# Kernel tuning notes

Hardware: AMD Instinct MI355X
Metric: run time of the kernel (lower is better)

The kernel has to match this reference:

```python
import jax, jax.numpy as jnp
import numpy as np

H = 128
NH = 8
HD = H // NH  # 16
TANH_ALPHA = 10.0
LN_EPS = 1e-5


def _layer_norm(x, g, b):
    mu = jnp.mean(x, axis=-1, keepdims=True)
    var = jnp.mean((x - mu) ** 2, axis=-1, keepdims=True)
    return (x - mu) / jnp.sqrt(var + LN_EPS) * g + b


def setup_inputs() -> dict:
    key = jax.random.key(0)
    ks = jax.random.split(key, 24)
    B, N = 1024, 500

    def p(k, shape):
        return jax.random.normal(k, shape, dtype=jnp.float32) * 0.05

    inp = {
        "node_embeddings": jax.random.normal(ks[0], (B, N, H), jnp.float32),
        "graph_embeddings": jax.random.normal(ks[1], (B, H), jnp.float32),
        "first_node": jax.random.randint(ks[2], (B,), 0, N, jnp.int32),
        "current_node": jax.random.randint(ks[3], (B,), 0, N, jnp.int32),
        "mask": jax.random.randint(ks[4], (B, N), 0, 2, jnp.int32),
        # linear_first: Linear(384, 128)
        "W_first": p(ks[5], (H, 3 * H)),
        "b_first": p(ks[6], (H,)),
        # ln1 / ln2
        "g1": jnp.ones((H,), jnp.float32),
        "beta1": jnp.zeros((H,), jnp.float32),
        "g2": jnp.ones((H,), jnp.float32),
        "beta2": jnp.zeros((H,), jnp.float32),
        # LSTM(128,128) single layer, gate order i,f,g,o
        "W_ih": p(ks[7], (4 * H, H)),
        "W_hh": p(ks[8], (4 * H, H)),
        "b_ih": p(ks[9], (4 * H,)),
        "b_hh": p(ks[10], (4 * H,)),
        # attention / output projections (no bias)
        "Wq": p(ks[11], (H, H)),
        "Wk": p(ks[12], (H, H)),
        "Wv": p(ks[13], (H, H)),
        "Wproj": p(ks[14], (H, H)),
        # logitk: Linear(128,128) with bias
        "Wlk": p(ks[15], (H, H)),
        "blk": p(ks[16], (H,)),
    }
    return inp


def reference(node_embeddings, graph_embeddings, W_first, b_first, g1, beta1,
              W_ih, W_hh, b_ih, b_hh, g2, beta2, Wq, Wk, Wv, Wproj, Wlk, blk,
              first_node, current_node, mask):
    B, N, _ = node_embeddings.shape
    dt = node_embeddings.dtype

    # build_cache: K/V/logitK projections of all node embeddings
    ck = node_embeddings @ Wk.T                # [B,N,128]
    cv = node_embeddings @ Wv.T                # [B,N,128]
    lk = node_embeddings @ Wlk.T + blk         # [B,N,128]

    # context construction
    bidx = jnp.arange(B)
    first_emb = node_embeddings[bidx, first_node]    # [B,128]
    cur_emb = node_embeddings[bidx, current_node]    # [B,128]
    context = jnp.concatenate([graph_embeddings, first_emb, cur_emb], axis=1)
    context = _layer_norm(context @ W_first.T + b_first, g1, beta1)

    # single LSTM step from zero state (build_cache resets h,c to 0)
    gates = context @ W_ih.T + b_ih + b_hh           # h_prev = 0 -> no W_hh term
    i, f, g, o = jnp.split(gates, 4, axis=-1)
    c = jax.nn.sigmoid(i) * jnp.tanh(g)              # c_prev = 0
    h = jax.nn.sigmoid(o) * jnp.tanh(c)
    ctx = _layer_norm(h, g2, beta2)

    # multi-head single-query attention; note (e h) split: head is the FAST dim
    q = (ctx @ Wq.T).reshape(B, HD, NH).transpose(0, 2, 1)       # [B,h,e]
    k = ck.reshape(B, N, HD, NH).transpose(0, 3, 1, 2)           # [B,h,N,e]
    v = cv.reshape(B, N, HD, NH).transpose(0, 3, 1, 2)           # [B,h,N,e]
    maskf = mask.astype(dt)
    scores = jnp.einsum('bhe,bhne->bhn', q, k) / np.sqrt(HD) + maskf[:, None, :]
    att = jax.nn.softmax(scores, axis=-1)
    oh = jnp.einsum('bhn,bhne->bhe', att, v)                     # [B,h,e]
    att_out = oh.reshape(B, H)                                   # (h e): h slow, e fast

    context_emb = att_out @ Wproj.T                              # [B,128]
    comp = jnp.einsum('be,bne->bn', lk, context_emb[:, None, :].squeeze(1)[:, :][None].squeeze(0) if False else context_emb) if False else jnp.einsum('bne,be->bn', lk, context_emb)
    comp = comp / np.sqrt(H)
    comp = TANH_ALPHA * jnp.tanh(comp)
    out = jnp.where(mask == 1, -jnp.inf, comp)
    return out
```

## Files before the change

### kernel.cpp

```cpp
#include <hip/hip_runtime.h>
#include <math.h>

#define NBATCH 1024
#define NNODE  500
#define HDIM   128
#define NHEAD  8
#define G1K    4
#define SPLIT  8
#define PSTRIDE 1040
#define RSQRT_H 0.08838834764831845f
#define MASK_NEG (-1e30f)

__device__ __forceinline__ float wave_sum64(float v) {
    #pragma unroll
    for (int off = 32; off >= 1; off >>= 1) v += __shfl_xor(v, off, 64);
    return v;
}
__device__ __forceinline__ float wave_max64(float v) {
    #pragma unroll
    for (int off = 32; off >= 1; off >>= 1) v = fmaxf(v, __shfl_xor(v, off, 64));
    return v;
}

template<int G>
__device__ __forceinline__ void block_ln(float (&x)[G], const float* __restrict__ gw,
                                         const float* __restrict__ bw,
                                         int t, int lane, int wv, float (*wpart)[G])
{
    float s[G];
    #pragma unroll
    for (int g = 0; g < G; ++g) s[g] = x[g];
    #pragma unroll
    for (int off = 32; off >= 1; off >>= 1) {
        #pragma unroll
        for (int g = 0; g < G; ++g) s[g] += __shfl_xor(s[g], off, 64);
    }
    if (lane == 0) {
        #pragma unroll
        for (int g = 0; g < G; ++g) wpart[wv][g] = s[g];
    }
    __syncthreads();
    float mu[G];
    #pragma unroll
    for (int g = 0; g < G; ++g) mu[g] = (wpart[0][g] + wpart[1][g]) * (1.f/128.f);
    __syncthreads();
    #pragma unroll
    for (int g = 0; g < G; ++g) { float d = x[g] - mu[g]; s[g] = d * d; }
    #pragma unroll
    for (int off = 32; off >= 1; off >>= 1) {
        #pragma unroll
        for (int g = 0; g < G; ++g) s[g] += __shfl_xor(s[g], off, 64);
    }
    if (lane == 0) {
        #pragma unroll
        for (int g = 0; g < G; ++g) wpart[wv][g] = s[g];
    }
    __syncthreads();
    float gv = gw[t], bv = bw[t];
    #pragma unroll
    for (int g = 0; g < G; ++g) {
        float var = (wpart[0][g] + wpart[1][g]) * (1.f/128.f);
        x[g] = (x[g] - mu[g]) / sqrtf(var + 1e-5f) * gv + bv;
    }
    __syncthreads();
}

__global__ __launch_bounds__(128) void k1_context(
    const float* __restrict__ node, const float* __restrict__ graph,
    const int* __restrict__ firstn, const int* __restrict__ curn,
    const float* __restrict__ W_first, const float* __restrict__ b_first,
    const float* __restrict__ g1, const float* __restrict__ beta1,
    const float* __restrict__ W_ih, const float* __restrict__ b_ih,
    const float* __restrict__ b_hh, const float* __restrict__ g2,
    const float* __restrict__ beta2, const float* __restrict__ Wq,
    const float* __restrict__ Wk, float* __restrict__ qW_out)
{
    const int t = threadIdx.x;
    const int lane = t & 63, wv = t >> 6;
    const int b0 = blockIdx.x * G1K;
    __shared__ __align__(16) float ctx[G1K][384];
    __shared__ __align__(16) float bufB[G1K][128];
    __shared__ float wpart[2][G1K];

    #pragma unroll
    for (int g = 0; g < G1K; ++g) {
        int b = b0 + g;
        ctx[g][t]       = graph[b*HDIM + t];
        ctx[g][128 + t] = node[((size_t)b*NNODE + firstn[b])*HDIM + t];
        ctx[g][256 + t] = node[((size_t)b*NNODE + curn[b])*HDIM + t];
    }
    __syncthreads();

    float x[G1K];
    {
        const float4* Wf4 = (const float4*)W_first;
        float bf = b_first[t];
        #pragma unroll
        for (int g = 0; g < G1K; ++g) x[g] = bf;
        for (int j4 = 0; j4 < 96; ++j4) {
            float4 w = Wf4[t*96 + j4];
            #pragma unroll
            for (int g = 0; g < G1K; ++g) {
                float4 c = ((const float4*)ctx[g])[j4];
                x[g] += c.x*w.x + c.y*w.y + c.z*w.z + c.w*w.w;
            }
        }
    }
    block_ln<G1K>(x, g1, beta1, t, lane, wv, wpart);

    #pragma unroll
    for (int g = 0; g < G1K; ++g) bufB[g][t] = x[g];
    __syncthreads();

    float gi[G1K], gg[G1K], go[G1K];
    {
        const float4* Wih4 = (const float4*)W_ih;
        float bi = b_ih[t]       + b_hh[t];
        float bg = b_ih[256 + t] + b_hh[256 + t];
        float bo = b_ih[384 + t] + b_hh[384 + t];
        #pragma unroll
        for (int g = 0; g < G1K; ++g) { gi[g] = bi; gg[g] = bg; go[g] = bo; }
        for (int j4 = 0; j4 < 32; ++j4) {
            float4 wi = Wih4[(size_t)t*32 + j4];
            float4 wg = Wih4[(size_t)(256 + t)*32 + j4];
            float4 wo = Wih4[(size_t)(384 + t)*32 + j4];
            #pragma unroll
            for (int g = 0; g < G1K; ++g) {
                float4 v = ((const float4*)bufB[g])[j4];
                gi[g] += v.x*wi.x + v.y*wi.y + v.z*wi.z + v.w*wi.w;
                gg[g] += v.x*wg.x + v.y*wg.y + v.z*wg.z + v.w*wg.w;
                go[g] += v.x*wo.x + v.y*wo.y + v.z*wo.z + v.w*wo.w;
            }
        }
    }
    #pragma unroll
    for (int g = 0; g < G1K; ++g) {
        float ig = 1.f / (1.f + expf(-gi[g]));
        float cc = ig * tanhf(gg[g]);
        float og = 1.f / (1.f + expf(-go[g]));
        x[g] = og * tanhf(cc);
    }
    block_ln<G1K>(x, g2, beta2, t, lane, wv, wpart);

    #pragma unroll
    for (int g = 0; g < G1K; ++g) bufB[g][t] = x[g];
    __syncthreads();

    float q8[G1K];
    #pragma unroll
    for (int g = 0; g < G1K; ++g) q8[g] = 0.f;
    {
        const float4* Wq4 = (const float4*)Wq;
        for (int j4 = 0; j4 < 32; ++j4) {
            float4 w = Wq4[t*32 + j4];
            #pragma unroll
            for (int g = 0; g < G1K; ++g) {
                float4 v = ((const float4*)bufB[g])[j4];
                q8[g] += v.x*w.x + v.y*w.y + v.z*w.z + v.w*w.w;
            }
        }
    }
    __syncthreads();
    #pragma unroll
    for (int g = 0; g < G1K; ++g) bufB[g][t] = q8[g];
    __syncthreads();

    for (int h = 0; h < NHEAD; ++h) {
        float a[G1K];
        #pragma unroll
        for (int g = 0; g < G1K; ++g) a[g] = 0.f;
        for (int e = 0; e < 16; ++e) {
            float w = Wk[(e*8 + h)*HDIM + t];
            #pragma unroll
            for (int g = 0; g < G1K; ++g) a[g] += bufB[g][e*8 + h] * w;
        }
        #pragma unroll
        for (int g = 0; g < G1K; ++g)
            qW_out[((size_t)(b0 + g)*NHEAD + h)*HDIM + t] = 0.25f * a[g];
    }
}

__global__ __launch_bounds__(256) void k2a_wave(
    const float* __restrict__ node, const int* __restrict__ mask,
    const float* __restrict__ qW, float* __restrict__ part)
{
    const int b   = blockIdx.x >> 3;
    const int s   = blockIdx.x & 7;
    const int tid = threadIdx.x;
    const int w   = tid >> 6;
    const int lane = tid & 63;
    const int rnl = lane >> 2;
    const int dq  = lane & 3;
    const int gn  = s*64 + w*16 + rnl;

    __shared__ __align__(16) float  s_qw[NHEAD*HDIM];
    __shared__ __align__(16) float4 s_tile[4][16*32];
    __shared__ float s_pp[4][NHEAD*16];
    __shared__ float s_ml[4][16];
    __shared__ float s_gml[16];

    ((float4*)s_qw)[tid] = ((const float4*)(qW + (size_t)b*NHEAD*HDIM))[tid];

    float4 R[8];
    float mf = 0.f;
    const bool valid = (gn < NNODE);
    if (valid) {
        const float4* src = (const float4*)(node + ((size_t)b*NNODE + gn)*HDIM) + dq*8;
        #pragma unroll
        for (int k = 0; k < 8; ++k) R[k] = src[k];
        mf = (float)mask[(size_t)b*NNODE + gn];
    } else {
        #pragma unroll
        for (int k = 0; k < 8; ++k) R[k] = make_float4(0.f,0.f,0.f,0.f);
    }
    __syncthreads();

    float sc[NHEAD];
    #pragma unroll
    for (int h = 0; h < NHEAD; ++h) {
        const float4* qh = (const float4*)(s_qw + h*HDIM) + dq*8;
        float t0 = 0.f;
        #pragma unroll
        for (int k = 0; k < 8; ++k) {
            float4 wv = qh[k];
            t0 += R[k].x*wv.x + R[k].y*wv.y + R[k].z*wv.z + R[k].w*wv.w;
        }
        sc[h] = t0;
    }
    #pragma unroll
    for (int h = 0; h < NHEAD; ++h) {
        sc[h] += __shfl_xor(sc[h], 1, 64);
        sc[h] += __shfl_xor(sc[h], 2, 64);
        sc[h] = valid ? sc[h] + mf : -INFINITY;
    }

    float m[NHEAD], l[NHEAD], p[NHEAD];
    #pragma unroll
    for (int h = 0; h < NHEAD; ++h) {
        float mx = sc[h];
        #pragma unroll
        for (int off = 4; off <= 32; off <<= 1) mx = fmaxf(mx, __shfl_xor(mx, off, 64));
        m[h] = mx;
        p[h] = __expf(sc[h] - mx);
        float sm = p[h];
        #pragma unroll
        for (int off = 4; off <= 32; off <<= 1) sm += __shfl_xor(sm, off, 64);
        l[h] = sm;
    }

    float4* tile = s_tile[w];
    #pragma unroll
    for (int k = 0; k < 8; ++k) {
        int q = dq*8 + k;
        tile[rnl*32 + (q ^ rnl)] = R[k];
    }
    if (dq == 0) {
        #pragma unroll
        for (int h = 0; h < NHEAD; ++h) s_pp[w][h*16 + rnl] = p[h];
    }
    if (lane == 0) {
        #pragma unroll
        for (int h = 0; h < NHEAD; ++h) { s_ml[w][h] = m[h]; s_ml[w][8 + h] = l[h]; }
    }

    float4 a4[4];
    #pragma unroll
    for (int j = 0; j < 4; ++j) a4[j] = make_float4(0.f,0.f,0.f,0.f);
    const int h2 = lane >> 3, d16 = lane & 7;
    #pragma unroll 4
    for (int r = 0; r < 16; ++r) {
        float pv = s_pp[w][h2*16 + r];
        #pragma unroll
        for (int j = 0; j < 4; ++j) {
            float4 nv = tile[r*32 + ((d16*4 + j) ^ r)];
            a4[j].x += pv*nv.x; a4[j].y += pv*nv.y;
            a4[j].z += pv*nv.z; a4[j].w += pv*nv.w;
        }
    }
    __syncthreads();

    if (tid < NHEAD) {
        float gm = -INFINITY;
        #pragma unroll
        for (int w4 = 0; w4 < 4; ++w4) gm = fmaxf(gm, s_ml[w4][tid]);
        float lm = 0.f;
        #pragma unroll
        for (int w4 = 0; w4 < 4; ++w4)
            lm += s_ml[w4][8 + tid] * __expf(s_ml[w4][tid] - gm);
        s_gml[tid] = gm; s_gml[8 + tid] = lm;
    }
    #pragma unroll
    for (int j = 0; j < 4; ++j)
        ((float4*)s_tile)[w*256 + h2*32 + d16*4 + j] = a4[j];
    __syncthreads();

    float* pbase = part + (size_t)blockIdx.x * PSTRIDE;
    {
        const int hh = tid >> 5;
        float gm = s_gml[hh];
        float4 tot = make_float4(0.f,0.f,0.f,0.f);
        #pragma unroll
        for (int w4 = 0; w4 < 4; ++w4) {
            float f = __expf(s_ml[w4][hh] - gm);
            float4 v = ((float4*)s_tile)[w4*256 + tid];
            tot.x += f*v.x; tot.y += f*v.y; tot.z += f*v.z; tot.w += f*v.w;
        }
        if (tid < 16) pbase[tid] = s_gml[tid];
        *(float4*)(pbase + 16 + tid*4) = tot;
    }
}

__global__ __launch_bounds__(256) void k2b_reduce(
    const float* __restrict__ part, const float* __restrict__ Wv,
    const float* __restrict__ Wproj, const float* __restrict__ Wlk,
    const float* __restrict__ blk, float* __restrict__ wce_out,
    float* __restrict__ bias_out)
{
    const int b = blockIdx.x;
    const int tid = threadIdx.x;
    __shared__ __align__(16) float s_an[NHEAD*HDIM];
    __shared__ float s_ao[HDIM], s_ce[HDIM];

    {
        const int h = tid >> 5, q = tid & 31;
        const float* pb = part + (size_t)b*SPLIT*PSTRIDE;
        float m[SPLIT], l[SPLIT];
        float gm = -INFINITY;
        #pragma unroll
        for (int s = 0; s < SPLIT; ++s) {
            m[s] = pb[s*PSTRIDE + h];
            l[s] = pb[s*PSTRIDE + 8 + h];
            gm = fmaxf(gm, m[s]);
        }
        float lsum = 0.f;
        float4 tot = make_float4(0.f,0.f,0.f,0.f);
        #pragma unroll
        for (int s = 0; s < SPLIT; ++s) {
            float f = __expf(m[s] - gm);
            lsum += l[s] * f;
            float4 v = *(const float4*)(pb + s*PSTRIDE + 16 + h*HDIM + q*4);
            tot.x += f*v.x; tot.y += f*v.y; tot.z += f*v.z; tot.w += f*v.w;
        }
        float inv = 1.f / lsum;
        tot.x *= inv; tot.y *= inv; tot.z *= inv; tot.w *= inv;
        *(float4*)(s_an + h*HDIM + q*4) = tot;
    }
    __syncthreads();

    if (tid < HDIM) {
        const int c = tid, h = c >> 4, e = c & 15;
        const int row = e*8 + h;
        float oh = 0.f;
        for (int d = 0; d < HDIM; ++d) oh += s_an[h*HDIM + d] * Wv[row*HDIM + d];
        s_ao[c] = oh;
    }
    __syncthreads();
    if (tid < HDIM) {
        const int c = tid;
        float ce = 0.f;
        for (int j = 0; j < HDIM; ++j) ce += s_ao[j] * Wproj[c*HDIM + j];
        s_ce[c] = ce;
    }
    __syncthreads();
    if (tid < HDIM) {
        const int d = tid;
        float w = 0.f;
        for (int c = 0; c < HDIM; ++c) w += s_ce[c] * Wlk[c*HDIM + d];
        wce_out[(size_t)b*HDIM + d] = w * RSQRT_H;
        if (d == 0) {
            float bb = 0.f;
            for (int c = 0; c < HDIM; ++c) bb += s_ce[c] * blk[c];
            bias_out[b] = bb * RSQRT_H;
        }
    }
}

__global__ __launch_bounds__(256) void k2_flash_mono(
    const float* __restrict__ node, const int* __restrict__ mask,
    const float* __restrict__ qW, const float* __restrict__ Wv,
    const float* __restrict__ Wproj, const float* __restrict__ Wlk,
    const float* __restrict__ blk, float* __restrict__ wce_out,
    float* __restrict__ bias_out)
{
    const int b = blockIdx.x;
    const int tid = threadIdx.x;
    const int lane = tid & 63;
    const int wave = tid >> 6;

    __shared__ float4 s_tile[64*32];
    __shared__ __align__(16) float s_qw[NHEAD*HDIM];
    __shared__ float  s_p[NHEAD*64];
    __shared__ float  s_m[NHEAD], s_l[NHEAD], s_c[NHEAD];
    __shared__ float  s_ao[HDIM], s_ce[HDIM];

    ((float4*)s_qw)[tid] = ((const float4*)(qW + (size_t)b*NHEAD*HDIM))[tid];
    if (tid < NHEAD) { s_m[tid] = -INFINITY; s_l[tid] = 0.f; }

    float4 acc[NHEAD];
    #pragma unroll
    for (int h = 0; h < NHEAD; ++h) acc[h] = make_float4(0.f,0.f,0.f,0.f);

    const int sn = tid & 63;
    const int hp = tid >> 6;
    const int sg = tid >> 5;
    const int aq = tid & 31;
    const float* nodeb = node + (size_t)b*NNODE*HDIM;

    for (int tile = 0; tile < 8; ++tile) {
        const int base = tile*64;
        #pragma unroll
        for (int i = 0; i < 8; ++i) {
            int idx = i*256 + tid;
            int r = idx >> 5, qq = idx & 31;
            int gn = base + r;
            float4 v = make_float4(0.f,0.f,0.f,0.f);
            if (gn < NNODE) v = *(const float4*)(nodeb + (size_t)gn*HDIM + qq*4);
            s_tile[r*32 + (qq ^ (r & 31))] = v;
        }
        __syncthreads();
        {
            float s0 = 0.f, s1 = 0.f;
            const int rb = sn*32, sw = sn & 31;
            const float4* qa = (const float4*)(s_qw + hp*HDIM);
            const float4* qb = (const float4*)(s_qw + (hp + 4)*HDIM);
            #pragma unroll 8
            for (int qq = 0; qq < 32; ++qq) {
                float4 nv = s_tile[rb + (qq ^ sw)];
                float4 av = qa[qq];
                float4 bv = qb[qq];
                s0 += nv.x*av.x + nv.y*av.y + nv.z*av.z + nv.w*av.w;
                s1 += nv.x*bv.x + nv.y*bv.y + nv.z*bv.z + nv.w*bv.w;
            }
            int gn = base + sn;
            if (gn < NNODE) {
                float mf = (float)mask[(size_t)b*NNODE + gn];
                s0 += mf; s1 += mf;
            } else { s0 = -INFINITY; s1 = -INFINITY; }
            s_p[hp*64 + sn] = s0;
            s_p[(hp + 4)*64 + sn] = s1;
        }
        __syncthreads();
        for (int hh = wave; hh < NHEAD; hh += 4) {
            float sv = s_p[hh*64 + lane];
            float mx = wave_max64(sv);
            float mO = s_m[hh];
            float mN = fmaxf(mO, mx);
            float pv = __expf(sv - mN);
            s_p[hh*64 + lane] = pv;
            float sm = wave_sum64(pv);
            if (lane == 0) {
                float corr = __expf(mO - mN);
                s_c[hh] = corr;
                s_l[hh] = s_l[hh]*corr + sm;
                s_m[hh] = mN;
            }
        }
        __syncthreads();
        {
            #pragma unroll
            for (int h = 0; h < NHEAD; ++h) {
                float c = s_c[h];
                acc[h].x *= c; acc[h].y *= c; acc[h].z *= c; acc[h].w *= c;
            }
            #pragma unroll
            for (int j = 0; j < 8; ++j) {
                int n = sg*8 + j;
                float4 nv = s_tile[n*32 + (aq ^ (n & 31))];
                #pragma unroll
                for (int h = 0; h < NHEAD; ++h) {
                    float p = s_p[h*64 + n];
                    acc[h].x += p*nv.x; acc[h].y += p*nv.y;
                    acc[h].z += p*nv.z; acc[h].w += p*nv.w;
                }
            }
        }
        __syncthreads();
    }
    #pragma unroll
    for (int h = 0; h < NHEAD; ++h) s_tile[(sg*8 + h)*32 + aq] = acc[h];
    __syncthreads();
    {
        const int h2 = tid >> 5, q2 = tid & 31;
        float4 tot = make_float4(0.f,0.f,0.f,0.f);
        #pragma unroll
        for (int s = 0; s < 8; ++s) {
            float4 v = s_tile[(s*8 + h2)*32 + q2];
            tot.x += v.x; tot.y += v.y; tot.z += v.z; tot.w += v.w;
        }
        float inv = 1.f / s_l[h2];
        tot.x *= inv; tot.y *= inv; tot.z *= inv; tot.w *= inv;
        ((float4*)s_qw)[h2*32 + q2] = tot;
    }
    __syncthreads();
    if (tid < HDIM) {
        const int c = tid, h = c >> 4, e = c & 15;
        const int row = e*8 + h;
        float oh = 0.f;
        for (int d = 0; d < HDIM; ++d) oh += s_qw[h*HDIM + d] * Wv[row*HDIM + d];
        s_ao[c] = oh;
    }
    __syncthreads();
    if (tid < HDIM) {
        const int c = tid;
        float ce = 0.f;
        for (int j = 0; j < HDIM; ++j) ce += s_ao[j] * Wproj[c*HDIM + j];
        s_ce[c] = ce;
    }
    __syncthreads();
    if (tid < HDIM) {
        const int d = tid;
        float w = 0.f;
        for (int c = 0; c < HDIM; ++c) w += s_ce[c] * Wlk[c*HDIM + d];
        wce_out[(size_t)b*HDIM + d] = w * RSQRT_H;
        if (d == 0) {
            float bb = 0.f;
            for (int c = 0; c < HDIM; ++c) bb += s_ce[c] * blk[c];
            bias_out[b] = bb * RSQRT_H;
        }
    }
}

__global__ __launch_bounds__(256) void k3_out(
    const float* __restrict__ node, const int* __restrict__ mask,
    const float* __restrict__ wce, const float* __restrict__ biasv,
    float* __restrict__ out)
{
    const int slot = (int)((blockIdx.x*256u + threadIdx.x) >> 5);
    const int q = threadIdx.x & 31;
    const int b = slot / NNODE;
    const float4 nv = *(const float4*)(node + (size_t)slot*HDIM + q*4);
    const float4 wv = *(const float4*)(wce + (size_t)b*HDIM + q*4);
    float p = nv.x*wv.x + nv.y*wv.y + nv.z*wv.z + nv.w*wv.w;
    #pragma unroll
    for (int off = 16; off >= 1; off >>= 1) p += __shfl_xor(p, off, 32);
    if (q == 0) {
        float v = 10.f * tanhf(p + biasv[b]);
        out[slot] = (mask[slot] == 1) ? MASK_NEG : v;
    }
}

extern "C" void kernel_launch(void* const* d_in, const int* in_sizes, int n_in,
                              void* d_out, int out_size, void* d_ws, size_t ws_size,
                              hipStream_t stream) {
    const float* node    = (const float*)d_in[0];
    const float* graph   = (const float*)d_in[1];
    const int*   firstn  = (const int*)d_in[2];
    const int*   curn    = (const int*)d_in[3];
    const int*   mask    = (const int*)d_in[4];
    const float* W_first = (const float*)d_in[5];
    const float* b_first = (const float*)d_in[6];
    const float* g1      = (const float*)d_in[7];
    const float* beta1   = (const float*)d_in[8];
    const float* g2      = (const float*)d_in[9];
    const float* beta2   = (const float*)d_in[10];
    const float* W_ih    = (const float*)d_in[11];
    const float* b_ih    = (const float*)d_in[13];
    const float* b_hh    = (const float*)d_in[14];
    const float* Wq      = (const float*)d_in[15];
    const float* Wk      = (const float*)d_in[16];
    const float* Wv      = (const float*)d_in[17];
    const float* Wproj   = (const float*)d_in[18];
    const float* Wlk     = (const float*)d_in[19];
    const float* blk     = (const float*)d_in[20];
    float* out = (float*)d_out;

    float* qW    = (float*)d_ws;
    float* wce   = qW + (size_t)NBATCH*NHEAD*HDIM;
    float* biasv = wce + (size_t)NBATCH*HDIM;
    float* part  = biasv + NBATCH;
    const size_t need = ((size_t)NBATCH*NHEAD*HDIM + (size_t)NBATCH*HDIM + NBATCH
                         + (size_t)NBATCH*SPLIT*PSTRIDE) * sizeof(float);

    k1_context<<<NBATCH/G1K, 128, 0, stream>>>(node, graph, firstn, curn,
        W_first, b_first, g1, beta1, W_ih, b_ih, b_hh, g2, beta2, Wq, Wk, qW);
    if (ws_size >= need) {
        k2a_wave<<<NBATCH*SPLIT, 256, 0, stream>>>(node, mask, qW, part);
        k2b_reduce<<<NBATCH, 256, 0, stream>>>(part, Wv, Wproj, Wlk, blk,
            wce, biasv);
    } else {
        k2_flash_mono<<<NBATCH, 256, 0, stream>>>(node, mask, qW, Wv, Wproj,
            Wlk, blk, wce, biasv);
    }
    k3_out<<<(NBATCH*NNODE)/8, 256, 0, stream>>>(node, mask, wce, biasv, out);
}
```

Measured before the change: 245.5 us.

## Split attention into score pass and bf16-copy softmax pass, reuse bf16 nodes in output

Replaces the split-flash attention with a kernel that computes per-head scores and also writes a bf16 copy of the node embeddings. A second kernel then does a full softmax over those scores and the weighted sum on the bf16 copy. The output kernel reads the bf16 copy instead of fp32 nodes. This aims to cut DRAM traffic in the later passes, at the cost of an extra write pass and reduced precision in the attention and output logits.

Result: slower. 313.9 us (+27.9%).

```diff
diff --git a/kernel.cpp b/kernel.cpp
--- a/kernel.cpp
+++ b/kernel.cpp
@@ -6,10 +6,16 @@
 #define HDIM   128
 #define NHEAD  8
 #define G1K    4
-#define SPLIT  8
-#define PSTRIDE 1040
 #define RSQRT_H 0.08838834764831845f
 #define MASK_NEG (-1e30f)
+
+__device__ __forceinline__ unsigned short bf16rne(float f) {
+    unsigned u = __float_as_uint(f);
+    return (unsigned short)((u + 0x7FFFu + ((u >> 16) & 1u)) >> 16);
+}
+__device__ __forceinline__ float bf2f(unsigned short u) {
+    return __uint_as_float(((unsigned)u) << 16);
+}
 
 __device__ __forceinline__ float wave_sum64(float v) {
     #pragma unroll
@@ -180,170 +186,137 @@
     }
 }
 
-__global__ __launch_bounds__(256) void k2a_wave(
+__global__ __launch_bounds__(256) void k2s_score(
     const float* __restrict__ node, const int* __restrict__ mask,
-    const float* __restrict__ qW, float* __restrict__ part)
-{
-    const int b   = blockIdx.x >> 3;
-    const int s   = blockIdx.x & 7;
+    const float* __restrict__ qW, float* __restrict__ scores,
+    unsigned short* __restrict__ nb16)
+{
+    const int blk = blockIdx.x;
+    const int b = blk >> 2;
+    const int qq = blk & 3;
     const int tid = threadIdx.x;
-    const int w   = tid >> 6;
-    const int lane = tid & 63;
-    const int rnl = lane >> 2;
-    const int dq  = lane & 3;
-    const int gn  = s*64 + w*16 + rnl;
-
-    __shared__ __align__(16) float  s_qw[NHEAD*HDIM];
-    __shared__ __align__(16) float4 s_tile[4][16*32];
-    __shared__ float s_pp[4][NHEAD*16];
-    __shared__ float s_ml[4][16];
-    __shared__ float s_gml[16];
+    const int g = tid >> 5, lane32 = tid & 31;
+    __shared__ __align__(16) float s_qw[NHEAD*HDIM];
 
     ((float4*)s_qw)[tid] = ((const float4*)(qW + (size_t)b*NHEAD*HDIM))[tid];
-
-    float4 R[8];
-    float mf = 0.f;
-    const bool valid = (gn < NNODE);
-    if (valid) {
-        const float4* src = (const float4*)(node + ((size_t)b*NNODE + gn)*HDIM) + dq*8;
-        #pragma unroll
-        for (int k = 0; k < 8; ++k) R[k] = src[k];
-        mf = (float)mask[(size_t)b*NNODE + gn];
-    } else {
-        #pragma unroll
-        for (int k = 0; k < 8; ++k) R[k] = make_float4(0.f,0.f,0.f,0.f);
-    }
-    __syncthreads();
-
-    float sc[NHEAD];
-    #pragma unroll
-    for (int h = 0; h < NHEAD; ++h) {
-        const float4* qh = (const float4*)(s_qw + h*HDIM) + dq*8;
-        float t0 = 0.f;
-        #pragma unroll
-        for (int k = 0; k < 8; ++k) {
-            float4 wv = qh[k];
-            t0 += R[k].x*wv.x + R[k].y*wv.y + R[k].z*wv.z + R[k].w*wv.w;
-        }
-        sc[h] = t0;
-    }
-    #pragma unroll
-    for (int h = 0; h < NHEAD; ++h) {
-        sc[h] += __shfl_xor(sc[h], 1, 64);
-        sc[h] += __shfl_xor(sc[h], 2, 64);
-        sc[h] = valid ? sc[h] + mf : -INFINITY;
-    }
-
-    float m[NHEAD], l[NHEAD], p[NHEAD];
-    #pragma unroll
-    for (int h = 0; h < NHEAD; ++h) {
-        float mx = sc[h];
-        #pragma unroll
-        for (int off = 4; off <= 32; off <<= 1) mx = fmaxf(mx, __shfl_xor(mx, off, 64));
-        m[h] = mx;
-        p[h] = __expf(sc[h] - mx);
-        float sm = p[h];
-        #pragma unroll
-        for (int off = 4; off <= 32; off <<= 1) sm += __shfl_xor(sm, off, 64);
-        l[h] = sm;
-    }
-
-    float4* tile = s_tile[w];
-    #pragma unroll
-    for (int k = 0; k < 8; ++k) {
-        int q = dq*8 + k;
-        tile[rnl*32 + (q ^ rnl)] = R[k];
-    }
-    if (dq == 0) {
-        #pragma unroll
-        for (int h = 0; h < NHEAD; ++h) s_pp[w][h*16 + rnl] = p[h];
-    }
-    if (lane == 0) {
-        #pragma unroll
-        for (int h = 0; h < NHEAD; ++h) { s_ml[w][h] = m[h]; s_ml[w][8 + h] = l[h]; }
-    }
-
-    float4 a4[4];
-    #pragma unroll
-    for (int j = 0; j < 4; ++j) a4[j] = make_float4(0.f,0.f,0.f,0.f);
-    const int h2 = lane >> 3, d16 = lane & 7;
-    #pragma unroll 4
-    for (int r = 0; r < 16; ++r) {
-        float pv = s_pp[w][h2*16 + r];
-        #pragma unroll
-        for (int j = 0; j < 4; ++j) {
-            float4 nv = tile[r*32 + ((d16*4 + j) ^ r)];
-            a4[j].x += pv*nv.x; a4[j].y += pv*nv.y;
-            a4[j].z += pv*nv.z; a4[j].w += pv*nv.w;
-        }
-    }
-    __syncthreads();
-
-    if (tid < NHEAD) {
-        float gm = -INFINITY;
-        #pragma unroll
-        for (int w4 = 0; w4 < 4; ++w4) gm = fmaxf(gm, s_ml[w4][tid]);
-        float lm = 0.f;
-        #pragma unroll
-        for (int w4 = 0; w4 < 4; ++w4)
-            lm += s_ml[w4][8 + tid] * __expf(s_ml[w4][tid] - gm);
-        s_gml[tid] = gm; s_gml[8 + tid] = lm;
-    }
-    #pragma unroll
-    for (int j = 0; j < 4; ++j)
-        ((float4*)s_tile)[w*256 + h2*32 + d16*4 + j] = a4[j];
-    __syncthreads();
-
-    float* pbase = part + (size_t)blockIdx.x * PSTRIDE;
-    {
-        const int hh = tid >> 5;
-        float gm = s_gml[hh];
-        float4 tot = make_float4(0.f,0.f,0.f,0.f);
-        #pragma unroll
-        for (int w4 = 0; w4 < 4; ++w4) {
-            float f = __expf(s_ml[w4][hh] - gm);
-            float4 v = ((float4*)s_tile)[w4*256 + tid];
-            tot.x += f*v.x; tot.y += f*v.y; tot.z += f*v.z; tot.w += f*v.w;
-        }
-        if (tid < 16) pbase[tid] = s_gml[tid];
-        *(float4*)(pbase + 16 + tid*4) = tot;
-    }
-}
-
-__global__ __launch_bounds__(256) void k2b_reduce(
-    const float* __restrict__ part, const float* __restrict__ Wv,
-    const float* __restrict__ Wproj, const float* __restrict__ Wlk,
-    const float* __restrict__ blk, float* __restrict__ wce_out,
-    float* __restrict__ bias_out)
-{
-    const int b = blockIdx.x;
-    const int tid = threadIdx.x;
+    __syncthreads();
+
+    const int nstart = qq * 125;
+    for (int it = 0; it < 16; ++it) {
+        int nl = it*8 + g;
+        if (nl < 125) {
+            int gn = nstart + nl;
+            size_t rbase = ((size_t)b*NNODE + gn)*32;
+            float4 nv = ((const float4*)node)[rbase + lane32];
+            float sc[8];
+            #pragma unroll
+            for (int h = 0; h < 8; ++h) {
+                float4 w = ((const float4*)s_qw)[h*32 + lane32];
+                sc[h] = nv.x*w.x + nv.y*w.y + nv.z*w.z + nv.w*w.w;
+            }
+            #pragma unroll
+            for (int off = 1; off <= 16; off <<= 1) {
+                #pragma unroll
+                for (int h = 0; h < 8; ++h) sc[h] += __shfl_xor(sc[h], off, 64);
+            }
+            float v = sc[0];
+            #pragma unroll
+            for (int h = 1; h < 8; ++h) v = ((lane32 & 7) == h) ? sc[h] : v;
+            if (lane32 < 8) {
+                float mf = (float)mask[(size_t)b*NNODE + gn];
+                scores[((size_t)b*NNODE + gn)*8 + lane32] = v + mf;
+            }
+            ushort4 u;
+            u.x = bf16rne(nv.x); u.y = bf16rne(nv.y);
+            u.z = bf16rne(nv.z); u.w = bf16rne(nv.w);
+            ((ushort4*)nb16)[rbase + lane32] = u;
+        }
+    }
+}
+
+__global__ __launch_bounds__(256) void k2w_attn(
+    const float* __restrict__ scores, const unsigned short* __restrict__ nb16,
+    const float* __restrict__ Wv, const float* __restrict__ Wproj,
+    const float* __restrict__ Wlk, const float* __restrict__ blk_,
+    float* __restrict__ wce_out, float* __restrict__ bias_out)
+{
+    const int b = blockIdx.x, tid = threadIdx.x;
+    const int lane = tid & 63, w = tid >> 6;
+    __shared__ __align__(16) float s_p[NNODE*NHEAD];
+    __shared__ float s_red[4][8];
+    __shared__ float s_m[8], s_l[8];
     __shared__ __align__(16) float s_an[NHEAD*HDIM];
     __shared__ float s_ao[HDIM], s_ce[HDIM];
 
     {
-        const int h = tid >> 5, q = tid & 31;
-        const float* pb = part + (size_t)b*SPLIT*PSTRIDE;
-        float m[SPLIT], l[SPLIT];
-        float gm = -INFINITY;
-        #pragma unroll
-        for (int s = 0; s < SPLIT; ++s) {
-            m[s] = pb[s*PSTRIDE + h];
-            l[s] = pb[s*PSTRIDE + 8 + h];
-            gm = fmaxf(gm, m[s]);
-        }
-        float lsum = 0.f;
-        float4 tot = make_float4(0.f,0.f,0.f,0.f);
-        #pragma unroll
-        for (int s = 0; s < SPLIT; ++s) {
-            float f = __expf(m[s] - gm);
-            lsum += l[s] * f;
-            float4 v = *(const float4*)(pb + s*PSTRIDE + 16 + h*HDIM + q*4);
-            tot.x += f*v.x; tot.y += f*v.y; tot.z += f*v.z; tot.w += f*v.w;
-        }
-        float inv = 1.f / lsum;
-        tot.x *= inv; tot.y *= inv; tot.z *= inv; tot.w *= inv;
-        *(float4*)(s_an + h*HDIM + q*4) = tot;
+        const float4* sc4 = (const float4*)(scores + (size_t)b*NNODE*NHEAD);
+        #pragma unroll
+        for (int i = 0; i < 4; ++i) {
+            int idx = i*256 + tid;
+            if (idx < 1000) ((float4*)s_p)[idx] = sc4[idx];
+        }
+    }
+    __syncthreads();
+    float mx[8];
+    #pragma unroll
+    for (int h = 0; h < 8; ++h) mx[h] = -INFINITY;
+    for (int r = tid; r < NNODE; r += 256) {
+        #pragma unroll
+        for (int h = 0; h < 8; ++h) mx[h] = fmaxf(mx[h], s_p[r*8 + h]);
+    }
+    #pragma unroll
+    for (int off = 1; off <= 32; off <<= 1) {
+        #pragma unroll
+        for (int h = 0; h < 8; ++h) mx[h] = fmaxf(mx[h], __shfl_xor(mx[h], off, 64));
+    }
+    if (lane == 0) {
+        #pragma unroll
+        for (int h = 0; h < 8; ++h) s_red[w][h] = mx[h];
+    }
+    __syncthreads();
+    if (tid < 8)
+        s_m[tid] = fmaxf(fmaxf(s_red[0][tid], s_red[1][tid]),
+                         fmaxf(s_red[2][tid], s_red[3][tid]));
+    __syncthreads();
+    float ls[8];
+    #pragma unroll
+    for (int h = 0; h < 8; ++h) ls[h] = 0.f;
+    for (int r = tid; r < NNODE; r += 256) {
+        #pragma unroll
+        for (int h = 0; h < 8; ++h) {
+            float p = __expf(s_p[r*8 + h] - s_m[h]);
+            s_p[r*8 + h] = p;
+            ls[h] += p;
+        }
+    }
+    #pragma unroll
+    for (int off = 1; off <= 32; off <<= 1) {
+        #pragma unroll
+        for (int h = 0; h < 8; ++h) ls[h] += __shfl_xor(ls[h], off, 64);
+    }
+    if (lane == 0) {
+        #pragma unroll
+        for (int h = 0; h < 8; ++h) s_red[w][h] = ls[h];
+    }
+    __syncthreads();
+    if (tid < 8)
+        s_l[tid] = s_red[0][tid] + s_red[1][tid] + s_red[2][tid] + s_red[3][tid];
+    __syncthreads();
+
+    const int h2 = tid >> 5, d8 = tid & 31;
+    float4 acc = make_float4(0.f, 0.f, 0.f, 0.f);
+    const ushort4* nb = (const ushort4*)nb16 + (size_t)b*NNODE*32 + d8;
+    #pragma unroll 4
+    for (int n = 0; n < NNODE; ++n) {
+        ushort4 u = nb[n*32];
+        float p = s_p[n*8 + h2];
+        acc.x += p * bf2f(u.x); acc.y += p * bf2f(u.y);
+        acc.z += p * bf2f(u.z); acc.w += p * bf2f(u.w);
+    }
+    {
+        float inv = 1.f / s_l[h2];
+        float4 o = make_float4(acc.x*inv, acc.y*inv, acc.z*inv, acc.w*inv);
+        *(float4*)(s_an + h2*HDIM + d8*4) = o;
     }
     __syncthreads();
 
@@ -364,14 +337,52 @@
     __syncthreads();
     if (tid < HDIM) {
         const int d = tid;
-        float w = 0.f;
-        for (int c = 0; c < HDIM; ++c) w += s_ce[c] * Wlk[c*HDIM + d];
-        wce_out[(size_t)b*HDIM + d] = w * RSQRT_H;
+        float wv2 = 0.f;
+        for (int c = 0; c < HDIM; ++c) wv2 += s_ce[c] * Wlk[c*HDIM + d];
+        wce_out[(size_t)b*HDIM + d] = wv2 * RSQRT_H;
         if (d == 0) {
             float bb = 0.f;
-            for (int c = 0; c < HDIM; ++c) bb += s_ce[c] * blk[c];
+            for (int c = 0; c < HDIM; ++c) bb += s_ce[c] * blk_[c];
             bias_out[b] = bb * RSQRT_H;
         }
+    }
+}
+
+__global__ __launch_bounds__(256) void k3_out_bf16(
+    const unsigned short* __restrict__ nb16, const int* __restrict__ mask,
+    const float* __restrict__ wce, const float* __restrict__ biasv,
+    float* __restrict__ out)
+{
+    const int slot = (int)((blockIdx.x*256u + threadIdx.x) >> 5);
+    const int q = threadIdx.x & 31;
+    const int b = slot / NNODE;
+    ushort4 u = ((const ushort4*)nb16)[(size_t)slot*32 + q];
+    const float4 wv = *(const float4*)(wce + (size_t)b*HDIM + q*4);
+    float p = bf2f(u.x)*wv.x + bf2f(u.y)*wv.y + bf2f(u.z)*wv.z + bf2f(u.w)*wv.w;
+    #pragma unroll
+    for (int off = 16; off >= 1; off >>= 1) p += __shfl_xor(p, off, 32);
+    if (q == 0) {
+        float v = 10.f * tanhf(p + biasv[b]);
+        out[slot] = (mask[slot] == 1) ? MASK_NEG : v;
+    }
+}
+
+__global__ __launch_bounds__(256) void k3_out_f32(
+    const float* __restrict__ node, const int* __restrict__ mask,
+    const float* __restrict__ wce, const float* __restrict__ biasv,
+    float* __restrict__ out)
+{
+    const int slot = (int)((blockIdx.x*256u + threadIdx.x) >> 5);
+    const int q = threadIdx.x & 31;
+    const int b = slot / NNODE;
+    const float4 nv = *(const float4*)(node + (size_t)slot*HDIM + q*4);
+    const float4 wv = *(const float4*)(wce + (size_t)b*HDIM + q*4);
+    float p = nv.x*wv.x + nv.y*wv.y + nv.z*wv.z + nv.w*wv.w;
+    #pragma unroll
+    for (int off = 16; off >= 1; off >>= 1) p += __shfl_xor(p, off, 32);
+    if (q == 0) {
+        float v = 10.f * tanhf(p + biasv[b]);
+        out[slot] = (mask[slot] == 1) ? MASK_NEG : v;
     }
 }
 
@@ -509,33 +520,14 @@
     __syncthreads();
     if (tid < HDIM) {
         const int d = tid;
-        float w = 0.f;
-        for (int c = 0; c < HDIM; ++c) w += s_ce[c] * Wlk[c*HDIM + d];
-        wce_out[(size_t)b*HDIM + d] = w * RSQRT_H;
+        float w2 = 0.f;
+        for (int c = 0; c < HDIM; ++c) w2 += s_ce[c] * Wlk[c*HDIM + d];
+        wce_out[(size_t)b*HDIM + d] = w2 * RSQRT_H;
         if (d == 0) {
             float bb = 0.f;
             for (int c = 0; c < HDIM; ++c) bb += s_ce[c] * blk[c];
             bias_out[b] = bb * RSQRT_H;
         }
-    }
-}
-
-__global__ __launch_bounds__(256) void k3_out(
-    const float* __restrict__ node, const int* __restrict__ mask,
-    const float* __restrict__ wce, const float* __restrict__ biasv,
-    float* __restrict__ out)
-{
-    const int slot = (int)((blockIdx.x*256u + threadIdx.x) >> 5);
-    const int q = threadIdx.x & 31;
-    const int b = slot / NNODE;
-    const float4 nv = *(const float4*)(node + (size_t)slot*HDIM + q*4);
-    const float4 wv = *(const float4*)(wce + (size_t)b*HDIM + q*4);
-    float p = nv.x*wv.x + nv.y*wv.y + nv.z*wv.z + nv.w*wv.w;
-    #pragma unroll
-    for (int off = 16; off >= 1; off >>= 1) p += __shfl_xor(p, off, 32);
-    if (q == 0) {
-        float v = 10.f * tanhf(p + biasv[b]);
-        out[slot] = (mask[slot] == 1) ? MASK_NEG : v;
     }
 }
 
@@ -564,22 +556,28 @@
     const float* blk     = (const float*)d_in[20];
     float* out = (float*)d_out;
 
-    float* qW    = (float*)d_ws;
-    float* wce   = qW + (size_t)NBATCH*NHEAD*HDIM;
-    float* biasv = wce + (size_t)NBATCH*HDIM;
-    float* part  = biasv + NBATCH;
+    float* qW     = (float*)d_ws;
+    float* wce    = qW + (size_t)NBATCH*NHEAD*HDIM;
+    float* biasv  = wce + (size_t)NBATCH*HDIM;
+    float* scores = biasv + NBATCH;
+    unsigned short* nb16 =
+        (unsigned short*)(scores + (size_t)NBATCH*NNODE*NHEAD);
     const size_t need = ((size_t)NBATCH*NHEAD*HDIM + (size_t)NBATCH*HDIM + NBATCH
-                         + (size_t)NBATCH*SPLIT*PSTRIDE) * sizeof(float);
+                         + (size_t)NBATCH*NNODE*NHEAD) * sizeof(float)
+                        + (size_t)NBATCH*NNODE*HDIM * sizeof(unsigned short);
 
     k1_context<<<NBATCH/G1K, 128, 0, stream>>>(node, graph, firstn, curn,
         W_first, b_first, g1, beta1, W_ih, b_ih, b_hh, g2, beta2, Wq, Wk, qW);
     if (ws_size >= need) {
-        k2a_wave<<<NBATCH*SPLIT, 256, 0, stream>>>(node, mask, qW, part);
-        k2b_reduce<<<NBATCH, 256, 0, stream>>>(part, Wv, Wproj, Wlk, blk,
+        k2s_score<<<NBATCH*4, 256, 0, stream>>>(node, mask, qW, scores, nb16);
+        k2w_attn<<<NBATCH, 256, 0, stream>>>(scores, nb16, Wv, Wproj, Wlk, blk,
             wce, biasv);
+        k3_out_bf16<<<(NBATCH*NNODE)/8, 256, 0, stream>>>(nb16, mask, wce,
+            biasv, out);
     } else {
         k2_flash_mono<<<NBATCH, 256, 0, stream>>>(node, mask, qW, Wv, Wproj,
             Wlk, blk, wce, biasv);
-    }
-    k3_out<<<(NBATCH*NNODE)/8, 256, 0, stream>>>(node, mask, wce, biasv, out);
-}
+        k3_out_f32<<<(NBATCH*NNODE)/8, 256, 0, stream>>>(node, mask, wce,
+            biasv, out);
+    }
+}
```
